# Optimization experiments

Measured on AMD Instinct MI355X. Metric: run time of the kernel, lower is better.

## Reference

```python
import jax, jax.numpy as jnp
import numpy as np

H = 32  # hidden size, fixed by the source module


def setup_inputs() -> dict:
    key = jax.random.key(0)
    ks = jax.random.split(key, 11)
    B, T = 1024, 999
    s = 0.1  # weight init scale
    return {
        "input": jax.random.normal(ks[0], (B, T), jnp.float32),
        "W_ih1": jax.random.normal(ks[1], (4 * H, 1), jnp.float32) * s,
        "W_hh1": jax.random.normal(ks[2], (4 * H, H), jnp.float32) * s,
        "b_ih1": jax.random.normal(ks[3], (4 * H,), jnp.float32) * s,
        "b_hh1": jax.random.normal(ks[4], (4 * H,), jnp.float32) * s,
        "W_ih2": jax.random.normal(ks[5], (4 * H, H), jnp.float32) * s,
        "W_hh2": jax.random.normal(ks[6], (4 * H, H), jnp.float32) * s,
        "b_ih2": jax.random.normal(ks[7], (4 * H,), jnp.float32) * s,
        "b_hh2": jax.random.normal(ks[8], (4 * H,), jnp.float32) * s,
        "W_lin": jax.random.normal(ks[9], (1, H), jnp.float32) * s,
        "b_lin": jax.random.normal(ks[10], (1,), jnp.float32) * s,
        "future": 1000,
    }


def _lstm_cell(x, h, c, W_ih, W_hh, b_ih, b_hh):
    # PyTorch LSTMCell: gates = x@W_ih^T + b_ih + h@W_hh^T + b_hh, order i,f,g,o
    z = x @ W_ih.T + h @ W_hh.T + (b_ih + b_hh)
    i, f, g, o = jnp.split(z, 4, axis=-1)
    c_new = jax.nn.sigmoid(f) * c + jax.nn.sigmoid(i) * jnp.tanh(g)
    h_new = jax.nn.sigmoid(o) * jnp.tanh(c_new)
    return h_new, c_new


def reference(input, W_ih1, W_hh1, b_ih1, b_hh1, W_ih2, W_hh2, b_ih2, b_hh2,
              W_lin, b_lin, future):
    B = input.shape[0]
    dt = input.dtype
    z = jnp.zeros((B, H), dt)

    def step_tf(carry, x_t):  # teacher-forced phase, x_t: [B]
        h1, c1, h2, c2 = carry
        h1, c1 = _lstm_cell(x_t[:, None], h1, c1, W_ih1, W_hh1, b_ih1, b_hh1)
        h2, c2 = _lstm_cell(h1, h2, c2, W_ih2, W_hh2, b_ih2, b_hh2)
        out = h2 @ W_lin.T + b_lin  # [B,1]
        return (h1, c1, h2, c2), out[:, 0]

    carry, outs1 = jax.lax.scan(step_tf, (z, z, z, z), input.T)  # outs1: [T,B]

    def step_gen(carry, _):
        h1, c1, h2, c2, out = carry
        h1, c1 = _lstm_cell(out, h1, c1, W_ih1, W_hh1, b_ih1, b_hh1)
        h2, c2 = _lstm_cell(h1, h2, c2, W_ih2, W_hh2, b_ih2, b_hh2)
        out = h2 @ W_lin.T + b_lin
        return (h1, c1, h2, c2, out), out[:, 0]

    last_out = outs1[-1][:, None]
    _, outs2 = jax.lax.scan(step_gen, (*carry, last_out), None, length=future)

    return jnp.concatenate([outs1, outs2], axis=0).T  # [B, T+future]
```

## Files before the change

kernel.cpp:

```cpp
#include <hip/hip_runtime.h>

#define HH 32
#define LOG2E 1.44269504088896340736f

typedef float v2f __attribute__((ext_vector_type(2)));

#define QP_XOR1 0xB1
#define QP_XOR2 0x4E
#define QP_XOR3 0x1B
#define QPERM(v, ctrl) \
    __int_as_float(__builtin_amdgcn_update_dpp(0, __float_as_int(v), (ctrl), 0xF, 0xF, true))

__device__ __forceinline__ float hw_exp2(float x) {
    float r;
    asm("v_exp_f32 %0, %1" : "=v"(r) : "v"(x));
    return r;
}
__device__ __forceinline__ float sigm_e(float z, float escale) {
    return __builtin_amdgcn_rcpf(1.0f + hw_exp2(z * escale));
}
__device__ __forceinline__ v2f pk_fma(v2f a, v2f b, v2f c) {
    return __builtin_elementwise_fma(a, b, c);
}

__global__ __launch_bounds__(128, 2)
void lstm_seq_kernel(const float* __restrict__ input,
                     const float* __restrict__ W_ih1, const float* __restrict__ W_hh1,
                     const float* __restrict__ b_ih1, const float* __restrict__ b_hh1,
                     const float* __restrict__ W_ih2, const float* __restrict__ W_hh2,
                     const float* __restrict__ b_ih2, const float* __restrict__ b_hh2,
                     const float* __restrict__ W_lin, const float* __restrict__ b_lin,
                     float* __restrict__ out, int T, int total)
{
    const int b    = blockIdx.x;
    const int tid  = threadIdx.x;
    const int w    = tid >> 6;
    const int lane = tid & 63;
    const int q    = lane & 3;
    const int m    = lane >> 2;
    const int j    = (w << 4) | m;
    const int row  = (q << 5) | j;

    __shared__ __align__(16) float h1buf[HH];
    __shared__ __align__(16) float h2buf[HH];

    v2f wh1v[16], wi2v[16], wh2v[16], wlv[16];
    {
        const v2f* p1 = (const v2f*)(W_hh1 + row * HH);
        const v2f* p2 = (const v2f*)(W_ih2 + row * HH);
        const v2f* p3 = (const v2f*)(W_hh2 + row * HH);
        const v2f* p4 = (const v2f*)(W_lin);
#pragma unroll
        for (int r = 0; r < 16; ++r) {
            wh1v[r] = p1[r]; wi2v[r] = p2[r]; wh2v[r] = p3[r]; wlv[r] = p4[r];
        }
    }
    const float wx   = W_ih1[row];
    const float b1   = b_ih1[row] + b_hh1[row];
    const float b2   = b_ih2[row] + b_hh2[row];
    const float blin = b_lin[0];

    const bool  isg = (q == 2);
    const float es  = isg ? (-2.0f * LOG2E) : (-LOG2E);
    const float mm  = isg ? 2.0f : 1.0f;
    const float cc  = isg ? -1.0f : 0.0f;

    float c1 = 0.0f, c2 = 0.0f;
    float ov = 0.0f;
    v2f a01 = {b1, 0.0f}, a23 = {0.0f, 0.0f};
    v2f e01 = {b2, 0.0f}, e23 = {0.0f, 0.0f};

    const float* __restrict__ inp  = input + (size_t)b * T;
    float* __restrict__       outp = out   + (size_t)b * total;

    for (int t = 0; t < total; ++t) {
        float xin = inp[t < T ? t : (T - 1)];
        float x   = (t < T) ? xin : ov;

        float z1  = fmaf(x, wx, (a01.x + a01.y) + (a23.x + a23.y));
        float act = fmaf(mm, sigm_e(z1, es), cc);
        float vf  = QPERM(act, QP_XOR1);
        float vg  = QPERM(act, QP_XOR2);
        float vo  = QPERM(act, QP_XOR3);
        c1 = fmaf(vf, c1, act * vg);
        float h1 = vo * fmaf(2.0f, sigm_e(c1, -2.0f * LOG2E), -1.0f);
        if (q == 0) h1buf[j] = h1;

        __syncthreads();

        v2f hv[16];
#pragma unroll
        for (int r = 0; r < 8; ++r) {
            float4 v = ((const float4*)h1buf)[r];
            hv[2*r]   = (v2f){v.x, v.y};
            hv[2*r+1] = (v2f){v.z, v.w};
        }
        a01 = (v2f){b1, 0.0f}; a23 = (v2f){0.0f, 0.0f};
#pragma unroll
        for (int r = 0; r < 16; r += 2) {
            e01 = pk_fma(hv[r],   wi2v[r],   e01);
            e23 = pk_fma(hv[r+1], wi2v[r+1], e23);
            a01 = pk_fma(hv[r],   wh1v[r],   a01);
            a23 = pk_fma(hv[r+1], wh1v[r+1], a23);
        }
        {
            float z2   = (e01.x + e01.y) + (e23.x + e23.y);
            float act2 = fmaf(mm, sigm_e(z2, es), cc);
            float vf2  = QPERM(act2, QP_XOR1);
            float vg2  = QPERM(act2, QP_XOR2);
            float vo2  = QPERM(act2, QP_XOR3);
            c2 = fmaf(vf2, c2, act2 * vg2);
            float h2 = vo2 * fmaf(2.0f, sigm_e(c2, -2.0f * LOG2E), -1.0f);
            if (q == 0) h2buf[j] = h2;
        }

        __syncthreads();

        v2f gv[16];
#pragma unroll
        for (int r = 0; r < 8; ++r) {
            float4 v = ((const float4*)h2buf)[r];
            gv[2*r]   = (v2f){v.x, v.y};
            gv[2*r+1] = (v2f){v.z, v.w};
        }
        e01 = (v2f){b2, 0.0f}; e23 = (v2f){0.0f, 0.0f};
        v2f o01 = {blin, 0.0f}, o23 = {0.0f, 0.0f};
#pragma unroll
        for (int r = 0; r < 16; r += 2) {
            e01 = pk_fma(gv[r],   wh2v[r],   e01);
            e23 = pk_fma(gv[r+1], wh2v[r+1], e23);
            o01 = pk_fma(gv[r],   wlv[r],    o01);
            o23 = pk_fma(gv[r+1], wlv[r+1],  o23);
        }
        ov = (o01.x + o01.y) + (o23.x + o23.y);
        if (tid == 0) outp[t] = ov;
    }
}

extern "C" void kernel_launch(void* const* d_in, const int* in_sizes, int n_in,
                              void* d_out, int out_size, void* d_ws, size_t ws_size,
                              hipStream_t stream) {
    const int B = 1024;
    const int T = in_sizes[0] / B;
    const int total = out_size / B;

    lstm_seq_kernel<<<dim3(B), dim3(128), 0, stream>>>(
        (const float*)d_in[0],
        (const float*)d_in[1], (const float*)d_in[2],
        (const float*)d_in[3], (const float*)d_in[4],
        (const float*)d_in[5], (const float*)d_in[6],
        (const float*)d_in[7], (const float*)d_in[8],
        (const float*)d_in[9], (const float*)d_in[10],
        (float*)d_out, T, total);
}
```

Before: 1.323 ms.

## Map one batch element per wavefront to drop block barriers

Each wavefront now owns a whole batch element and computes two hidden units per lane group (rows A and B), so the h1/h2 exchange through LDS stays inside one wave and the two __syncthreads per step are removed. The block size grows to 256 threads holding 4 elements, and the grid shrinks by 4x. The recurrent matvecs are reordered so the output projection and next-step products sit off the critical path, and the next input is prefetched one step ahead. In exchange, each lane holds twice as many weight registers, which lowers occupancy. The code also relies on implicit wave-level ordering of LDS writes and reads with no explicit barrier.

```diff
diff --git a/kernel.cpp b/kernel.cpp
--- a/kernel.cpp
+++ b/kernel.cpp
@@ -12,18 +12,24 @@
     __int_as_float(__builtin_amdgcn_update_dpp(0, __float_as_int(v), (ctrl), 0xF, 0xF, true))
 
 __device__ __forceinline__ float hw_exp2(float x) {
-    float r;
-    asm("v_exp_f32 %0, %1" : "=v"(r) : "v"(x));
-    return r;
+    float r; asm("v_exp_f32 %0, %1" : "=v"(r) : "v"(x)); return r;
 }
-__device__ __forceinline__ float sigm_e(float z, float escale) {
-    return __builtin_amdgcn_rcpf(1.0f + hw_exp2(z * escale));
+__device__ __forceinline__ float sigm_e(float z, float e) {
+    return __builtin_amdgcn_rcpf(1.0f + hw_exp2(z * e));
 }
 __device__ __forceinline__ v2f pk_fma(v2f a, v2f b, v2f c) {
     return __builtin_elementwise_fma(a, b, c);
 }
+__device__ __forceinline__ void load_bc(const float* p, v2f* d) {
+#pragma unroll
+    for (int r = 0; r < 8; ++r) {
+        float4 v = ((const float4*)p)[r];
+        d[2*r]   = (v2f){v.x, v.y};
+        d[2*r+1] = (v2f){v.z, v.w};
+    }
+}
 
-__global__ __launch_bounds__(128, 2)
+__global__ __launch_bounds__(256, 1)
 void lstm_seq_kernel(const float* __restrict__ input,
                      const float* __restrict__ W_ih1, const float* __restrict__ W_hh1,
                      const float* __restrict__ b_ih1, const float* __restrict__ b_hh1,
@@ -32,32 +38,41 @@
                      const float* __restrict__ W_lin, const float* __restrict__ b_lin,
                      float* __restrict__ out, int T, int total)
 {
-    const int b    = blockIdx.x;
     const int tid  = threadIdx.x;
     const int w    = tid >> 6;
     const int lane = tid & 63;
+    const int e    = blockIdx.x * 4 + w;
     const int q    = lane & 3;
-    const int m    = lane >> 2;
-    const int j    = (w << 4) | m;
-    const int row  = (q << 5) | j;
+    const int c    = lane >> 2;
+    const int rowA = (q << 5) | c;
+    const int rowB = (q << 5) | (c + 16);
 
-    __shared__ __align__(16) float h1buf[HH];
-    __shared__ __align__(16) float h2buf[HH];
+    __shared__ __align__(16) float lds[4][64];
+    float* h1buf = &lds[w][0];
+    float* h2buf = &lds[w][32];
 
-    v2f wh1v[16], wi2v[16], wh2v[16], wlv[16];
+    v2f wh1A[16], wh1B[16], wi2A[16], wi2B[16], wh2A[16], wh2B[16], wlv[16];
     {
-        const v2f* p1 = (const v2f*)(W_hh1 + row * HH);
-        const v2f* p2 = (const v2f*)(W_ih2 + row * HH);
-        const v2f* p3 = (const v2f*)(W_hh2 + row * HH);
-        const v2f* p4 = (const v2f*)(W_lin);
+        const v2f* a1 = (const v2f*)(W_hh1 + rowA * HH);
+        const v2f* b1p = (const v2f*)(W_hh1 + rowB * HH);
+        const v2f* a2 = (const v2f*)(W_ih2 + rowA * HH);
+        const v2f* b2p = (const v2f*)(W_ih2 + rowB * HH);
+        const v2f* a3 = (const v2f*)(W_hh2 + rowA * HH);
+        const v2f* b3p = (const v2f*)(W_hh2 + rowB * HH);
+        const v2f* pl = (const v2f*)(W_lin);
 #pragma unroll
         for (int r = 0; r < 16; ++r) {
-            wh1v[r] = p1[r]; wi2v[r] = p2[r]; wh2v[r] = p3[r]; wlv[r] = p4[r];
+            wh1A[r] = a1[r]; wh1B[r] = b1p[r];
+            wi2A[r] = a2[r]; wi2B[r] = b2p[r];
+            wh2A[r] = a3[r]; wh2B[r] = b3p[r];
+            wlv[r]  = pl[r];
         }
     }
-    const float wx   = W_ih1[row];
-    const float b1   = b_ih1[row] + b_hh1[row];
-    const float b2   = b_ih2[row] + b_hh2[row];
+    const float wxA = W_ih1[rowA], wxB = W_ih1[rowB];
+    const float b1A = b_ih1[rowA] + b_hh1[rowA];
+    const float b1B = b_ih1[rowB] + b_hh1[rowB];
+    const float b2A = b_ih2[rowA] + b_hh2[rowA];
+    const float b2B = b_ih2[rowB] + b_hh2[rowB];
     const float blin = b_lin[0];
 
     const bool  isg = (q == 2);
@@ -65,75 +80,86 @@
     const float mm  = isg ? 2.0f : 1.0f;
     const float cc  = isg ? -1.0f : 0.0f;
 
-    float c1 = 0.0f, c2 = 0.0f;
+    float c1A = 0.f, c1B = 0.f, c2A = 0.f, c2B = 0.f;
     float ov = 0.0f;
-    v2f a01 = {b1, 0.0f}, a23 = {0.0f, 0.0f};
-    v2f e01 = {b2, 0.0f}, e23 = {0.0f, 0.0f};
+    v2f aA0 = {b1A, 0.f}, aA1 = {0.f, 0.f};
+    v2f aB0 = {b1B, 0.f}, aB1 = {0.f, 0.f};
+    v2f eA0 = {b2A, 0.f}, eA1 = {0.f, 0.f};
+    v2f eB0 = {b2B, 0.f}, eB1 = {0.f, 0.f};
 
-    const float* __restrict__ inp  = input + (size_t)b * T;
-    float* __restrict__       outp = out   + (size_t)b * total;
+    const float* __restrict__ inp  = input + (size_t)e * T;
+    float* __restrict__       outp = out   + (size_t)e * total;
+    float xcur = inp[0];
 
     for (int t = 0; t < total; ++t) {
-        float xin = inp[t < T ? t : (T - 1)];
-        float x   = (t < T) ? xin : ov;
+        float x = (t < T) ? xcur : ov;
+        int tn = t + 1;
+        xcur = inp[tn < T ? tn : (T - 1)];
 
-        float z1  = fmaf(x, wx, (a01.x + a01.y) + (a23.x + a23.y));
-        float act = fmaf(mm, sigm_e(z1, es), cc);
-        float vf  = QPERM(act, QP_XOR1);
-        float vg  = QPERM(act, QP_XOR2);
-        float vo  = QPERM(act, QP_XOR3);
-        c1 = fmaf(vf, c1, act * vg);
-        float h1 = vo * fmaf(2.0f, sigm_e(c1, -2.0f * LOG2E), -1.0f);
-        if (q == 0) h1buf[j] = h1;
+        float z1A = fmaf(x, wxA, (aA0.x + aA0.y) + (aA1.x + aA1.y));
+        float z1B = fmaf(x, wxB, (aB0.x + aB0.y) + (aB1.x + aB1.y));
+        float acA = fmaf(mm, sigm_e(z1A, es), cc);
+        float acB = fmaf(mm, sigm_e(z1B, es), cc);
+        float fA = QPERM(acA, QP_XOR1), gA = QPERM(acA, QP_XOR2), oA = QPERM(acA, QP_XOR3);
+        float fB = QPERM(acB, QP_XOR1), gB = QPERM(acB, QP_XOR2), oB = QPERM(acB, QP_XOR3);
+        c1A = fmaf(fA, c1A, acA * gA);
+        c1B = fmaf(fB, c1B, acB * gB);
+        float h1A = oA * fmaf(2.0f, sigm_e(c1A, -2.0f * LOG2E), -1.0f);
+        float h1B = oB * fmaf(2.0f, sigm_e(c1B, -2.0f * LOG2E), -1.0f);
+        if (q == 0) { h1buf[c] = h1A; h1buf[c + 16] = h1B; }
 
-        __syncthreads();
+        v2f h1v[16]; load_bc(h1buf, h1v);
 
-        v2f hv[16];
-#pragma unroll
-        for (int r = 0; r < 8; ++r) {
-            float4 v = ((const float4*)h1buf)[r];
-            hv[2*r]   = (v2f){v.x, v.y};
-            hv[2*r+1] = (v2f){v.z, v.w};
-        }
-        a01 = (v2f){b1, 0.0f}; a23 = (v2f){0.0f, 0.0f};
+        v2f sA0 = eA0, sA1 = eA1, sB0 = eB0, sB1 = eB1;
 #pragma unroll
         for (int r = 0; r < 16; r += 2) {
-            e01 = pk_fma(hv[r],   wi2v[r],   e01);
-            e23 = pk_fma(hv[r+1], wi2v[r+1], e23);
-            a01 = pk_fma(hv[r],   wh1v[r],   a01);
-            a23 = pk_fma(hv[r+1], wh1v[r+1], a23);
+            sA0 = pk_fma(h1v[r],   wi2A[r],   sA0);
+            sA1 = pk_fma(h1v[r+1], wi2A[r+1], sA1);
+            sB0 = pk_fma(h1v[r],   wi2B[r],   sB0);
+            sB1 = pk_fma(h1v[r+1], wi2B[r+1], sB1);
         }
-        {
-            float z2   = (e01.x + e01.y) + (e23.x + e23.y);
-            float act2 = fmaf(mm, sigm_e(z2, es), cc);
-            float vf2  = QPERM(act2, QP_XOR1);
-            float vg2  = QPERM(act2, QP_XOR2);
-            float vo2  = QPERM(act2, QP_XOR3);
-            c2 = fmaf(vf2, c2, act2 * vg2);
-            float h2 = vo2 * fmaf(2.0f, sigm_e(c2, -2.0f * LOG2E), -1.0f);
-            if (q == 0) h2buf[j] = h2;
+        float z2A = (sA0.x + sA0.y) + (sA1.x + sA1.y);
+        float z2B = (sB0.x + sB0.y) + (sB1.x + sB1.y);
+        float dcA = fmaf(mm, sigm_e(z2A, es), cc);
+        float dcB = fmaf(mm, sigm_e(z2B, es), cc);
+        float fA2 = QPERM(dcA, QP_XOR1), gA2 = QPERM(dcA, QP_XOR2), oA2 = QPERM(dcA, QP_XOR3);
+        float fB2 = QPERM(dcB, QP_XOR1), gB2 = QPERM(dcB, QP_XOR2), oB2 = QPERM(dcB, QP_XOR3);
+        c2A = fmaf(fA2, c2A, dcA * gA2);
+        c2B = fmaf(fB2, c2B, dcB * gB2);
+        float h2A = oA2 * fmaf(2.0f, sigm_e(c2A, -2.0f * LOG2E), -1.0f);
+        float h2B = oB2 * fmaf(2.0f, sigm_e(c2B, -2.0f * LOG2E), -1.0f);
+        if (q == 0) { h2buf[c] = h2A; h2buf[c + 16] = h2B; }
+
+        aA0 = (v2f){b1A, 0.f}; aA1 = (v2f){0.f, 0.f};
+        aB0 = (v2f){b1B, 0.f}; aB1 = (v2f){0.f, 0.f};
+#pragma unroll
+        for (int r = 0; r < 16; r += 2) {
+            aA0 = pk_fma(h1v[r],   wh1A[r],   aA0);
+            aA1 = pk_fma(h1v[r+1], wh1A[r+1], aA1);
+            aB0 = pk_fma(h1v[r],   wh1B[r],   aB0);
+            aB1 = pk_fma(h1v[r+1], wh1B[r+1], aB1);
         }
 
-        __syncthreads();
+        v2f h2v[16]; load_bc(h2buf, h2v);
 
-        v2f gv[16];
-#pragma unroll
-        for (int r = 0; r < 8; ++r) {
-            float4 v = ((const float4*)h2buf)[r];
-            gv[2*r]   = (v2f){v.x, v.y};
-            gv[2*r+1] = (v2f){v.z, v.w};
-        }
-        e01 = (v2f){b2, 0.0f}; e23 = (v2f){0.0f, 0.0f};
-        v2f o01 = {blin, 0.0f}, o23 = {0.0f, 0.0f};
+        v2f o0 = {blin, 0.f}, o1 = {0.f, 0.f};
 #pragma unroll
         for (int r = 0; r < 16; r += 2) {
-            e01 = pk_fma(gv[r],   wh2v[r],   e01);
-            e23 = pk_fma(gv[r+1], wh2v[r+1], e23);
-            o01 = pk_fma(gv[r],   wlv[r],    o01);
-            o23 = pk_fma(gv[r+1], wlv[r+1],  o23);
+            o0 = pk_fma(h2v[r],   wlv[r],   o0);
+            o1 = pk_fma(h2v[r+1], wlv[r+1], o1);
         }
-        ov = (o01.x + o01.y) + (o23.x + o23.y);
-        if (tid == 0) outp[t] = ov;
+        ov = (o0.x + o0.y) + (o1.x + o1.y);
+        if (lane == 0) outp[t] = ov;
+
+        eA0 = (v2f){b2A, 0.f}; eA1 = (v2f){0.f, 0.f};
+        eB0 = (v2f){b2B, 0.f}; eB1 = (v2f){0.f, 0.f};
+#pragma unroll
+        for (int r = 0; r < 16; r += 2) {
+            eA0 = pk_fma(h2v[r],   wh2A[r],   eA0);
+            eA1 = pk_fma(h2v[r+1], wh2A[r+1], eA1);
+            eB0 = pk_fma(h2v[r],   wh2B[r],   eB0);
+            eB1 = pk_fma(h2v[r+1], wh2B[r+1], eB1);
+        }
     }
 }
 
@@ -144,7 +170,7 @@
     const int T = in_sizes[0] / B;
     const int total = out_size / B;
 
-    lstm_seq_kernel<<<dim3(B), dim3(128), 0, stream>>>(
+    lstm_seq_kernel<<<dim3(B / 4), dim3(256), 0, stream>>>(
         (const float*)d_in[0],
         (const float*)d_in[1], (const float*)d_in[2],
         (const float*)d_in[3], (const float*)d_in[4],
```

Result: slower. 1.442 ms (+9.0%).
